# Kernel optimization log

Measured on AMD Instinct MI355X. Metric: run time of the kernel, lower is better.

Reference implementation:

```python
import jax, jax.numpy as jnp
import numpy as np

N = 65536   # number of points
K = 32      # num_centroid
D = 64      # x_width


def setup_inputs() -> dict:
    key = jax.random.key(0)
    k1, k2 = jax.random.split(key)
    input_x = jax.random.normal(k1, (N, D), dtype=jnp.float32)
    input_centroid = jax.random.normal(k2, (K, D), dtype=jnp.float32)
    return {"input_x": input_x, "input_centroid": input_centroid}


def reference(input_x, input_centroid):
    # expanded_centroid: [K, 1, D]; expanded_point: [1, N, D]
    # test = expanded_point - expanded_centroid -> [K, N, D]
    diff = input_x[None, :, :] - input_centroid[:, None, :]
    return diff
```

## Files before the change

### kernel.cpp

```cpp
#include <hip/hip_runtime.h>


#define NPTS 65536
#define KC   32
#define DW   64
#define D4   (DW / 4)

__global__ __launch_bounds__(256) void kmeans_diff_kernel(
    const float4* __restrict__ x,
    const float4* __restrict__ c,
    float4* __restrict__ out)
{
    const int tid = blockIdx.x * blockDim.x + threadIdx.x;
    const int d4  = tid & (D4 - 1);

    const float4 xv = x[tid];

    const int plane = NPTS * D4;

#pragma unroll
    for (int k = 0; k < KC; ++k) {
        const float4 cv = c[k * D4 + d4];
        float4 o;
        o.x = xv.x - cv.x;
        o.y = xv.y - cv.y;
        o.z = xv.z - cv.z;
        o.w = xv.w - cv.w;
        out[k * plane + tid] = o;
    }
}

extern "C" void kernel_launch(void* const* d_in, const int* in_sizes, int n_in,
                              void* d_out, int out_size, void* d_ws, size_t ws_size,
                              hipStream_t stream) {
    const float4* x = (const float4*)d_in[0];
    const float4* c = (const float4*)d_in[1];
    float4* out = (float4*)d_out;

    const int total_threads = NPTS * D4;
    const int block = 256;
    const int grid = total_threads / block;

    kmeans_diff_kernel<<<grid, block, 0, stream>>>(x, c, out);
}
```

Before: 546.5 us.

## Reindex over output with one centroid per thread and nontemporal stores

The work mapping is reorganized so each block writes a contiguous chunk of the output. Each thread holds one centroid vector and streams 8 strided x vectors, instead of each thread looping over all 32 centroids and writing to 32 planes 4 MB apart. Output stores use nontemporal hints to avoid polluting cache with the 512 MB write stream. The cost is that x is re-read 32 times, though these reads should mostly hit in cache.

```diff
diff --git a/kernel.cpp b/kernel.cpp
--- a/kernel.cpp
+++ b/kernel.cpp
@@ -3,43 +3,44 @@
 
 #define NPTS 65536
 #define KC   32
-#define DW   64
-#define D4   (DW / 4)
+#define D4   16
+#define PLANE (NPTS * D4)
+#define PER_THREAD 8
+#define BLOCK 256
+#define CHUNK (BLOCK * PER_THREAD)
 
-__global__ __launch_bounds__(256) void kmeans_diff_kernel(
-    const float4* __restrict__ x,
-    const float4* __restrict__ c,
-    float4* __restrict__ out)
+typedef float f4 __attribute__((ext_vector_type(4)));
+
+__global__ __launch_bounds__(BLOCK) void kmeans_diff_kernel(
+    const f4* __restrict__ x,
+    const f4* __restrict__ c,
+    f4* __restrict__ out)
 {
-    const int tid = blockIdx.x * blockDim.x + threadIdx.x;
-    const int d4  = tid & (D4 - 1);
+    const int base = blockIdx.x * CHUNK + threadIdx.x;
 
-    const float4 xv = x[tid];
+    const int k   = base >> 20;
+    const int d4  = base & (D4 - 1);
+    const int idx0 = base & (PLANE - 1);
 
-    const int plane = NPTS * D4;
+    const f4 cv = c[(k << 4) | d4];
 
 #pragma unroll
-    for (int k = 0; k < KC; ++k) {
-        const float4 cv = c[k * D4 + d4];
-        float4 o;
-        o.x = xv.x - cv.x;
-        o.y = xv.y - cv.y;
-        o.z = xv.z - cv.z;
-        o.w = xv.w - cv.w;
-        out[k * plane + tid] = o;
+    for (int t = 0; t < PER_THREAD; ++t) {
+        const f4 xv = x[idx0 + t * BLOCK];
+        const f4 o  = xv - cv;
+        __builtin_nontemporal_store(o, &out[base + t * BLOCK]);
     }
 }
 
 extern "C" void kernel_launch(void* const* d_in, const int* in_sizes, int n_in,
                               void* d_out, int out_size, void* d_ws, size_t ws_size,
                               hipStream_t stream) {
-    const float4* x = (const float4*)d_in[0];
-    const float4* c = (const float4*)d_in[1];
-    float4* out = (float4*)d_out;
+    const f4* x = reinterpret_cast<const f4*>(d_in[0]);
+    const f4* c = reinterpret_cast<const f4*>(d_in[1]);
+    f4* out = reinterpret_cast<f4*>(d_out);
 
-    const int total_threads = NPTS * D4;
-    const int block = 256;
-    const int grid = total_threads / block;
+    const int total = KC * PLANE;
+    const int grid = total / CHUNK;
 
-    kmeans_diff_kernel<<<grid, block, 0, stream>>>(x, c, out);
+    kmeans_diff_kernel<<<grid, BLOCK, 0, stream>>>(x, c, out);
 }
```

After: 528.3 us. -3.3%, faster.
